# Kernel optimization log

Hardware: AMD Instinct MI355X
Metric: run time of the kernel (lower is better)

## Reference

```python
import jax, jax.numpy as jnp
import numpy as np

# Static feature-pyramid shapes (stride 8/16/32 of a 512x512 image)
SPATIAL_SHAPES = ((64, 64), (32, 32), (16, 16))
SEQ = sum(h * w for h, w in SPATIAL_SHAPES)  # 5376
B, D, NH, NL, NP = 4, 256, 8, 3, 4
DH = D // NH  # 32


def _reference_points():
    # normalized pixel centers per level, valid_ratios == 1
    refs = []
    for (h, w) in SPATIAL_SHAPES:
        ry = (jnp.arange(h, dtype=jnp.float32) + 0.5) / h
        rx = (jnp.arange(w, dtype=jnp.float32) + 0.5) / w
        yy, xx = jnp.meshgrid(ry, rx, indexing='ij')
        refs.append(jnp.stack([xx.reshape(-1), yy.reshape(-1)], -1))  # [h*w, 2]
    ref = jnp.concatenate(refs, 0)  # [S, 2]
    return jnp.broadcast_to(ref[None, :, None, :], (B, SEQ, NL, 2))


def setup_inputs() -> dict:
    key = jax.random.key(0)
    ks = jax.random.split(key, 8)
    s = 0.02
    return {
        'hidden_states': jax.random.normal(ks[0], (B, SEQ, D), jnp.float32),
        'position_embeddings': jax.random.normal(ks[1], (B, SEQ, D), jnp.float32),
        'reference_points': _reference_points(),
        'Wv': jax.random.normal(ks[2], (D, D), jnp.float32) * s,
        'bv': jnp.zeros((D,), jnp.float32),
        'Wo': jax.random.normal(ks[3], (D, NH * NL * NP * 2), jnp.float32) * s,
        'bo': jax.random.normal(ks[4], (NH * NL * NP * 2,), jnp.float32) * 0.1,
        'Wa': jax.random.normal(ks[5], (D, NH * NL * NP), jnp.float32) * s,
        'ba': jnp.zeros((NH * NL * NP,), jnp.float32),
        'Wout': jax.random.normal(ks[6], (D, D), jnp.float32) * s,
        'bout': jnp.zeros((D,), jnp.float32),
    }


def _bilinear_sample(img, gx, gy):
    # img: [N, C, H, W]; gx, gy: [N, Q, P] in [-1, 1]
    # grid_sample(mode='bilinear', padding_mode='zeros', align_corners=False)
    N, C, H, W = img.shape
    x = (gx + 1.0) * (W * 0.5) - 0.5
    y = (gy + 1.0) * (H * 0.5) - 0.5
    x0 = jnp.floor(x)
    y0 = jnp.floor(y)
    wx, wy = x - x0, y - y0
    flat = img.reshape(N, C, H * W)
    out = jnp.zeros((N, C) + gx.shape[1:], img.dtype)
    for xi, wxi in ((x0, 1.0 - wx), (x0 + 1.0, wx)):
        for yi, wyi in ((y0, 1.0 - wy), (y0 + 1.0, wy)):
            valid = (xi >= 0) & (xi < W) & (yi >= 0) & (yi < H)
            xc = jnp.clip(xi, 0, W - 1).astype(jnp.int32)
            yc = jnp.clip(yi, 0, H - 1).astype(jnp.int32)
            idx = (yc * W + xc).reshape(N, 1, -1)  # [N,1,Q*P]
            v = jnp.take_along_axis(flat, idx, axis=2).reshape(N, C, *gx.shape[1:])
            out = out + v * (wxi * wyi * valid.astype(img.dtype))[:, None]
    return out  # [N, C, Q, P]


def reference(hidden_states, position_embeddings, reference_points,
              Wv, bv, Wo, bo, Wa, ba, Wout, bout):
    hs = hidden_states + position_embeddings  # queries carry pos embed
    value = hidden_states @ Wv + bv           # value from raw encoder states
    value = value.reshape(B, SEQ, NH, DH)

    off = (hs @ Wo + bo).reshape(B, SEQ, NH, NL, NP, 2)
    attn = jax.nn.softmax((hs @ Wa + ba).reshape(B, SEQ, NH, NL * NP), -1)
    attn = attn.reshape(B, SEQ, NH, NL, NP)

    # offset normalizer: [W_l, H_l] per level
    norm = jnp.array([[w, h] for (h, w) in SPATIAL_SHAPES], jnp.float32)
    loc = reference_points[:, :, None, :, None, :] + off / norm[None, None, None, :, None, :]
    grid = 2.0 * loc - 1.0  # [B, Q, H, L, P, 2]

    sampled = []
    start = 0
    for lvl, (h, w) in enumerate(SPATIAL_SHAPES):
        v_l = value[:, start:start + h * w]  # [B, h*w, H, d]
        start += h * w
        v_l = v_l.transpose(0, 2, 3, 1).reshape(B * NH, DH, h, w)
        g_l = grid[:, :, :, lvl].transpose(0, 2, 1, 3, 4).reshape(B * NH, SEQ, NP, 2)
        sampled.append(_bilinear_sample(v_l, g_l[..., 0], g_l[..., 1]))  # [B*H,d,Q,P]
    sampled = jnp.stack(sampled, -2).reshape(B * NH, DH, SEQ, NL * NP)

    aw = attn.transpose(0, 2, 1, 3, 4).reshape(B * NH, 1, SEQ, NL * NP)
    out = (sampled * aw).sum(-1)                   # [B*H, d, Q]
    out = out.reshape(B, NH * DH, SEQ).transpose(0, 2, 1)  # [B, Q, D]
    out = out @ Wout + bout
    return out, attn
```

## Files before the change

### kernel.cpp

```cpp
#include <hip/hip_runtime.h>
#include <hip/hip_bf16.h>
#include <math.h>

#define BB 4
#define SEQ 5376
#define DD 256
#define NH 8
#define NL 3
#define NP 4
#define DH 32
#define MTOT (BB * SEQ)

typedef __attribute__((ext_vector_type(8))) short bf16x8;
typedef __attribute__((ext_vector_type(4))) float f32x4;

__device__ __forceinline__ ushort f2b(float f) {
    __hip_bfloat16 h = __float2bfloat16(f);
    return *reinterpret_cast<ushort*>(&h);
}

__global__ void prep_acts(const float4* __restrict__ h, const float4* __restrict__ p,
                          ushort4* __restrict__ hb, ushort4* __restrict__ hsb, int n4) {
    int i = blockIdx.x * blockDim.x + threadIdx.x;
    int stride = gridDim.x * blockDim.x;
    for (; i < n4; i += stride) {
        float4 a = h[i], b = p[i];
        ushort4 ua, us;
        ua.x = f2b(a.x); ua.y = f2b(a.y); ua.z = f2b(a.z); ua.w = f2b(a.w);
        us.x = f2b(a.x + b.x); us.y = f2b(a.y + b.y);
        us.z = f2b(a.z + b.z); us.w = f2b(a.w + b.w);
        hb[i] = ua;
        hsb[i] = us;
    }
}

__global__ __launch_bounds__(256) void prep_w(
    const float* __restrict__ Wv, const float* __restrict__ Wo,
    const float* __restrict__ Wa, const float* __restrict__ Wout,
    const float* __restrict__ bo, const float* __restrict__ ba,
    ushort* __restrict__ Wt, float* __restrict__ bcomb) {
    int row = blockIdx.x;
    int k = threadIdx.x;
    if (row == 800) {
        for (int i = k; i < 288; i += 256)
            bcomb[i] = (i < 192) ? bo[i] : ba[i - 192];
        return;
    }
    const float* src;
    int N, n;
    if (row < 256)      { src = Wv;   N = 256; n = row; }
    else if (row < 448) { src = Wo;   N = 192; n = row - 256; }
    else if (row < 544) { src = Wa;   N = 96;  n = row - 448; }
    else                { src = Wout; N = 256; n = row - 544; }
    float v = src[(size_t)k * N + n];
    Wt[(size_t)row * 256 + k] = f2b(v);
}

template<bool OBF>
__global__ __launch_bounds__(256) void gemm_mfma(
    const ushort* __restrict__ A, const ushort* __restrict__ Wt,
    const float* __restrict__ bias, void* __restrict__ Cout,
    int M, int N, int K) {
    const int BM = 128, BN = 64, BK = 64, PK = 72;
    __shared__ ushort As[BM][PK];
    __shared__ ushort Bs[BN][PK];
    int bm = blockIdx.y * BM;
    int bn = blockIdx.x * BN;
    int tid = threadIdx.x;
    int lane = tid & 63;
    int wid = tid >> 6;
    int wr = wid >> 1, wc = wid & 1;
    int lr = lane & 15;
    int kg = lane >> 4;

    f32x4 acc[4][2] = {};

    for (int k0 = 0; k0 < K; k0 += BK) {
        #pragma unroll
        for (int c = 0; c < 4; c++) {
            int e = tid + 256 * c;
            int row = e >> 3, q = e & 7;
            const ushort* src = A + (size_t)(bm + row) * K + k0 + 8 * q;
            *(bf16x8*)&As[row][8 * q] = *(const bf16x8*)src;
        }
        #pragma unroll
        for (int c = 0; c < 2; c++) {
            int e = tid + 256 * c;
            int row = e >> 3, q = e & 7;
            int gn = bn + row;
            bf16x8 v = {0, 0, 0, 0, 0, 0, 0, 0};
            if (gn < N) v = *(const bf16x8*)(Wt + (size_t)gn * K + k0 + 8 * q);
            *(bf16x8*)&Bs[row][8 * q] = v;
        }
        __syncthreads();
        #pragma unroll
        for (int ks = 0; ks < 2; ks++) {
            bf16x8 af[4], bfr[2];
            #pragma unroll
            for (int mf = 0; mf < 4; mf++)
                af[mf] = *(bf16x8*)&As[wr * 64 + mf * 16 + lr][ks * 32 + kg * 8];
            #pragma unroll
            for (int nf = 0; nf < 2; nf++)
                bfr[nf] = *(bf16x8*)&Bs[wc * 32 + nf * 16 + lr][ks * 32 + kg * 8];
            #pragma unroll
            for (int mf = 0; mf < 4; mf++)
                #pragma unroll
                for (int nf = 0; nf < 2; nf++)
                    acc[mf][nf] = __builtin_amdgcn_mfma_f32_16x16x32_bf16(
                        af[mf], bfr[nf], acc[mf][nf], 0, 0, 0);
        }
        __syncthreads();
    }

    #pragma unroll
    for (int nf = 0; nf < 2; nf++) {
        int gc = bn + wc * 32 + nf * 16 + lr;
        if (gc >= N) continue;
        float bv = bias[gc];
        #pragma unroll
        for (int mf = 0; mf < 4; mf++) {
            int gr0 = bm + wr * 64 + mf * 16 + kg * 4;
            #pragma unroll
            for (int r = 0; r < 4; r++) {
                float v = acc[mf][nf][r] + bv;
                if constexpr (OBF)
                    ((ushort*)Cout)[(size_t)(gr0 + r) * N + gc] = f2b(v);
                else
                    ((float*)Cout)[(size_t)(gr0 + r) * N + gc] = v;
            }
        }
    }
}

struct Acc8 {
    float a0, a1, a2, a3, a4, a5, a6, a7;
};

__device__ __forceinline__ void fma8(Acc8& acc, float wt, uint4 u) {
    acc.a0 = fmaf(wt, __uint_as_float(u.x << 16), acc.a0);
    acc.a1 = fmaf(wt, __uint_as_float(u.x & 0xffff0000u), acc.a1);
    acc.a2 = fmaf(wt, __uint_as_float(u.y << 16), acc.a2);
    acc.a3 = fmaf(wt, __uint_as_float(u.y & 0xffff0000u), acc.a3);
    acc.a4 = fmaf(wt, __uint_as_float(u.z << 16), acc.a4);
    acc.a5 = fmaf(wt, __uint_as_float(u.z & 0xffff0000u), acc.a5);
    acc.a6 = fmaf(wt, __uint_as_float(u.w << 16), acc.a6);
    acc.a7 = fmaf(wt, __uint_as_float(u.w & 0xffff0000u), acc.a7);
}

__global__ __launch_bounds__(128) void msda_sample_v7(
    const ushort* __restrict__ value, const float* __restrict__ comb,
    const float* __restrict__ refp, float* __restrict__ attn_out,
    ushort* __restrict__ out) {
    __shared__ int4   s_idx[4][8][13];
    __shared__ float4 s_w[4][8][13];
    int tid = threadIdx.x;
    int bq0 = blockIdx.x * 4;

    #pragma unroll
    for (int it = 0; it < 4; it++) {
        int t = tid + it * 128;
        int lp = t & 15;
        int qh = t >> 4;
        int q = qh >> 3, h = qh & 7;
        int bq = bq0 + q;
        bool active = lp < 12;
        const float* crow = comb + (size_t)bq * 288;
        float logit = active ? crow[192 + h * 12 + lp] : -INFINITY;
        float m = logit;
        m = fmaxf(m, __shfl_xor(m, 1, 16));
        m = fmaxf(m, __shfl_xor(m, 2, 16));
        m = fmaxf(m, __shfl_xor(m, 4, 16));
        m = fmaxf(m, __shfl_xor(m, 8, 16));
        float e = active ? expf(logit - m) : 0.f;
        float s = e;
        s += __shfl_xor(s, 1, 16);
        s += __shfl_xor(s, 2, 16);
        s += __shfl_xor(s, 4, 16);
        s += __shfl_xor(s, 8, 16);
        float aw = e / s;
        if (active) {
            attn_out[(size_t)bq * 96 + h * 12 + lp] = aw;
            int l = lp >> 2;
            int b = bq / SEQ;
            int Wl = 64 >> l;
            float fW = (float)Wl;
            float rx = refp[(size_t)bq * 6 + 2 * l];
            float ry = refp[(size_t)bq * 6 + 2 * l + 1];
            float ox = crow[h * 24 + lp * 2];
            float oy = crow[h * 24 + lp * 2 + 1];
            float x = rx * fW + ox - 0.5f;
            float y = ry * fW + oy - 0.5f;
            float x0f = floorf(x), y0f = floorf(y);
            float wx = x - x0f, wy = y - y0f;
            int x0 = (int)x0f, y0 = (int)y0f;
            int x1 = x0 + 1, y1 = y0 + 1;
            float vx0 = (x0 >= 0 && x0 < Wl) ? 1.f : 0.f;
            float vx1 = (x1 >= 0 && x1 < Wl) ? 1.f : 0.f;
            float vy0 = (y0 >= 0 && y0 < Wl) ? 1.f : 0.f;
            float vy1 = (y1 >= 0 && y1 < Wl) ? 1.f : 0.f;
            int xc0 = min(max(x0, 0), Wl - 1);
            int xc1 = min(max(x1, 0), Wl - 1);
            int yc0 = min(max(y0, 0), Wl - 1);
            int yc1 = min(max(y1, 0), Wl - 1);
            int st = (l == 0) ? 0 : ((l == 1) ? 4096 : 5120);
            int rowbase = b * SEQ + st;
            s_idx[q][h][lp] = make_int4((rowbase + yc0 * Wl + xc0) << 8,
                                        (rowbase + yc0 * Wl + xc1) << 8,
                                        (rowbase + yc1 * Wl + xc0) << 8,
                                        (rowbase + yc1 * Wl + xc1) << 8);
            s_w[q][h][lp] = make_float4(aw * (1.f - wx) * (1.f - wy) * vx0 * vy0,
                                        aw * wx * (1.f - wy) * vx1 * vy0,
                                        aw * (1.f - wx) * wy * vx0 * vy1,
                                        aw * wx * wy * vx1 * vy1);
        }
    }
    __syncthreads();

    int wave = tid >> 6, lane = tid & 63;
    int q2 = lane >> 5;
    int lane5 = lane & 31;
    int h = lane5 >> 2, d8 = lane5 & 3;
    int q = wave * 2 + q2;
    int bq = bq0 + q;
    int ch0 = h * 32 + d8 * 8;
    const ushort* vb = value + ch0;

    Acc8 acc = {0.f, 0.f, 0.f, 0.f, 0.f, 0.f, 0.f, 0.f};
    #pragma unroll
    for (int lp = 0; lp < 12; lp++) {
        int4 ii = s_idx[q][h][lp];
        float4 ww = s_w[q][h][lp];
        uint4 u0 = *(const uint4*)(vb + ii.x);
        uint4 u1 = *(const uint4*)(vb + ii.y);
        uint4 u2 = *(const uint4*)(vb + ii.z);
        uint4 u3 = *(const uint4*)(vb + ii.w);
        fma8(acc, ww.x, u0);
        fma8(acc, ww.y, u1);
        fma8(acc, ww.z, u2);
        fma8(acc, ww.w, u3);
    }

    bf16x8 o;
    o[0] = (short)f2b(acc.a0); o[1] = (short)f2b(acc.a1);
    o[2] = (short)f2b(acc.a2); o[3] = (short)f2b(acc.a3);
    o[4] = (short)f2b(acc.a4); o[5] = (short)f2b(acc.a5);
    o[6] = (short)f2b(acc.a6); o[7] = (short)f2b(acc.a7);
    *(bf16x8*)(out + (size_t)bq * 256 + ch0) = o;
}

extern "C" void kernel_launch(void* const* d_in, const int* in_sizes, int n_in,
                              void* d_out, int out_size, void* d_ws, size_t ws_size,
                              hipStream_t stream) {
    const float* hidden = (const float*)d_in[0];
    const float* pos    = (const float*)d_in[1];
    const float* refp   = (const float*)d_in[2];
    const float* Wv     = (const float*)d_in[3];
    const float* bv     = (const float*)d_in[4];
    const float* Wo     = (const float*)d_in[5];
    const float* bo     = (const float*)d_in[6];
    const float* Wa     = (const float*)d_in[7];
    const float* ba     = (const float*)d_in[8];
    const float* Wout   = (const float*)d_in[9];
    const float* bout   = (const float*)d_in[10];

    float* out      = (float*)d_out;
    float* attn_out = out + (size_t)BB * SEQ * DD;

    const size_t BSD = (size_t)BB * SEQ * DD;
    char* w = (char*)d_ws;
    ushort* value_bf = (ushort*)w;  w += BSD * 2;
    float*  comb     = (float*)w;   w += (size_t)MTOT * 288 * 4;
    ushort* sampb    = (ushort*)w;  w += BSD * 2;
    ushort* hb       = (ushort*)w;  w += BSD * 2;
    ushort* hsb      = (ushort*)w;  w += BSD * 2;
    ushort* Wt       = (ushort*)w;  w += (size_t)800 * 256 * 2;
    float*  bcomb    = (float*)w;

    {
        int n4 = (int)(BSD / 4);
        prep_acts<<<2048, 256, 0, stream>>>((const float4*)hidden, (const float4*)pos,
                                            (ushort4*)hb, (ushort4*)hsb, n4);
    }
    prep_w<<<801, 256, 0, stream>>>(Wv, Wo, Wa, Wout, bo, ba, Wt, bcomb);

    const ushort* Wv_t    = Wt;
    const ushort* Wcomb_t = Wt + (size_t)256 * 256;
    const ushort* Wout_t  = Wt + (size_t)544 * 256;

    {
        dim3 grid(DD / 64, MTOT / 128);
        gemm_mfma<true><<<grid, 256, 0, stream>>>(hb, Wv_t, bv, value_bf, MTOT, DD, DD);
    }
    {
        dim3 grid(5, MTOT / 128);
        gemm_mfma<false><<<grid, 256, 0, stream>>>(hsb, Wcomb_t, bcomb, comb, MTOT, 288, DD);
    }
    {
        msda_sample_v7<<<MTOT / 4, 128, 0, stream>>>(value_bf, comb, refp,
                                                     attn_out, sampb);
    }
    {
        dim3 grid(DD / 64, MTOT / 128);
        gemm_mfma<false><<<grid, 256, 0, stream>>>(sampb, Wout_t, bout, out, MTOT, DD, DD);
    }
}
```

Before: 94.18 us.

## Merge prep kernels, widen GEMM N-tile to 128, shrink sampler blocks

Merges the activation and weight conversion kernels into one launch, splitting the work by block index. The GEMM N-tile grows from 64 to 128, so each wave holds 4x4 MFMA accumulators and more output shares each A-tile load. The sampling kernel now uses single-wave 64-thread blocks that each handle two queries instead of four. Together these remove a launch and improve A-tile reuse, but the GEMMs launch fewer blocks, which use more registers, and the combined GEMM (N=288) wastes part of its third column tile.

Result: no change. 94.98 us (+0.8%).

```diff
diff --git a/kernel.cpp b/kernel.cpp
--- a/kernel.cpp
+++ b/kernel.cpp
@@ -19,12 +19,38 @@
     return *reinterpret_cast<ushort*>(&h);
 }
 
-__global__ void prep_acts(const float4* __restrict__ h, const float4* __restrict__ p,
-                          ushort4* __restrict__ hb, ushort4* __restrict__ hsb, int n4) {
-    int i = blockIdx.x * blockDim.x + threadIdx.x;
-    int stride = gridDim.x * blockDim.x;
+__global__ __launch_bounds__(256) void prep_all(
+    const float* __restrict__ hidden, const float* __restrict__ pos,
+    const float* __restrict__ Wv, const float* __restrict__ Wo,
+    const float* __restrict__ Wa, const float* __restrict__ Wout,
+    const float* __restrict__ bo, const float* __restrict__ ba,
+    ushort4* __restrict__ hb, ushort4* __restrict__ hsb,
+    ushort* __restrict__ Wt, float* __restrict__ bcomb, int n4) {
+    int bid = blockIdx.x;
+    int tid = threadIdx.x;
+    if (bid <= 800) {
+        if (bid == 800) {
+            for (int i = tid; i < 288; i += 256)
+                bcomb[i] = (i < 192) ? bo[i] : ba[i - 192];
+            return;
+        }
+        int row = bid;
+        const float* src;
+        int N, n;
+        if (row < 256)      { src = Wv;   N = 256; n = row; }
+        else if (row < 448) { src = Wo;   N = 192; n = row - 256; }
+        else if (row < 544) { src = Wa;   N = 96;  n = row - 448; }
+        else                { src = Wout; N = 256; n = row - 544; }
+        float v = src[(size_t)tid * N + n];
+        Wt[(size_t)row * 256 + tid] = f2b(v);
+        return;
+    }
+    const float4* h4 = (const float4*)hidden;
+    const float4* p4 = (const float4*)pos;
+    int i = (bid - 801) * 256 + tid;
+    int stride = (gridDim.x - 801) * 256;
     for (; i < n4; i += stride) {
-        float4 a = h[i], b = p[i];
+        float4 a = h4[i], b = p4[i];
         ushort4 ua, us;
         ua.x = f2b(a.x); ua.y = f2b(a.y); ua.z = f2b(a.z); ua.w = f2b(a.w);
         us.x = f2b(a.x + b.x); us.y = f2b(a.y + b.y);
@@ -34,34 +60,12 @@
     }
 }
 
-__global__ __launch_bounds__(256) void prep_w(
-    const float* __restrict__ Wv, const float* __restrict__ Wo,
-    const float* __restrict__ Wa, const float* __restrict__ Wout,
-    const float* __restrict__ bo, const float* __restrict__ ba,
-    ushort* __restrict__ Wt, float* __restrict__ bcomb) {
-    int row = blockIdx.x;
-    int k = threadIdx.x;
-    if (row == 800) {
-        for (int i = k; i < 288; i += 256)
-            bcomb[i] = (i < 192) ? bo[i] : ba[i - 192];
-        return;
-    }
-    const float* src;
-    int N, n;
-    if (row < 256)      { src = Wv;   N = 256; n = row; }
-    else if (row < 448) { src = Wo;   N = 192; n = row - 256; }
-    else if (row < 544) { src = Wa;   N = 96;  n = row - 448; }
-    else                { src = Wout; N = 256; n = row - 544; }
-    float v = src[(size_t)k * N + n];
-    Wt[(size_t)row * 256 + k] = f2b(v);
-}
-
 template<bool OBF>
 __global__ __launch_bounds__(256) void gemm_mfma(
     const ushort* __restrict__ A, const ushort* __restrict__ Wt,
     const float* __restrict__ bias, void* __restrict__ Cout,
     int M, int N, int K) {
-    const int BM = 128, BN = 64, BK = 64, PK = 72;
+    const int BM = 128, BN = 128, BK = 64, PK = 72;
     __shared__ ushort As[BM][PK];
     __shared__ ushort Bs[BN][PK];
     int bm = blockIdx.y * BM;
@@ -73,7 +77,7 @@
     int lr = lane & 15;
     int kg = lane >> 4;
 
-    f32x4 acc[4][2] = {};
+    f32x4 acc[4][4] = {};
 
     for (int k0 = 0; k0 < K; k0 += BK) {
         #pragma unroll
@@ -84,7 +88,7 @@
             *(bf16x8*)&As[row][8 * q] = *(const bf16x8*)src;
         }
         #pragma unroll
-        for (int c = 0; c < 2; c++) {
+        for (int c = 0; c < 4; c++) {
             int e = tid + 256 * c;
             int row = e >> 3, q = e & 7;
             int gn = bn + row;
@@ -95,17 +99,17 @@
         __syncthreads();
         #pragma unroll
         for (int ks = 0; ks < 2; ks++) {
-            bf16x8 af[4], bfr[2];
+            bf16x8 af[4], bfr[4];
             #pragma unroll
             for (int mf = 0; mf < 4; mf++)
                 af[mf] = *(bf16x8*)&As[wr * 64 + mf * 16 + lr][ks * 32 + kg * 8];
             #pragma unroll
-            for (int nf = 0; nf < 2; nf++)
-                bfr[nf] = *(bf16x8*)&Bs[wc * 32 + nf * 16 + lr][ks * 32 + kg * 8];
+            for (int nf = 0; nf < 4; nf++)
+                bfr[nf] = *(bf16x8*)&Bs[wc * 64 + nf * 16 + lr][ks * 32 + kg * 8];
             #pragma unroll
             for (int mf = 0; mf < 4; mf++)
                 #pragma unroll
-                for (int nf = 0; nf < 2; nf++)
+                for (int nf = 0; nf < 4; nf++)
                     acc[mf][nf] = __builtin_amdgcn_mfma_f32_16x16x32_bf16(
                         af[mf], bfr[nf], acc[mf][nf], 0, 0, 0);
         }
@@ -113,8 +117,8 @@
     }
 
     #pragma unroll
-    for (int nf = 0; nf < 2; nf++) {
-        int gc = bn + wc * 32 + nf * 16 + lr;
+    for (int nf = 0; nf < 4; nf++) {
+        int gc = bn + wc * 64 + nf * 16 + lr;
         if (gc >= N) continue;
         float bv = bias[gc];
         #pragma unroll
@@ -147,18 +151,18 @@
     acc.a7 = fmaf(wt, __uint_as_float(u.w & 0xffff0000u), acc.a7);
 }
 
-__global__ __launch_bounds__(128) void msda_sample_v7(
+__global__ __launch_bounds__(64) void msda_sample_v8(
     const ushort* __restrict__ value, const float* __restrict__ comb,
     const float* __restrict__ refp, float* __restrict__ attn_out,
     ushort* __restrict__ out) {
-    __shared__ int4   s_idx[4][8][13];
-    __shared__ float4 s_w[4][8][13];
+    __shared__ int4   s_idx[2][8][13];
+    __shared__ float4 s_w[2][8][13];
     int tid = threadIdx.x;
-    int bq0 = blockIdx.x * 4;
+    int bq0 = blockIdx.x * 2;
 
     #pragma unroll
     for (int it = 0; it < 4; it++) {
-        int t = tid + it * 128;
+        int t = tid + it * 64;
         int lp = t & 15;
         int qh = t >> 4;
         int q = qh >> 3, h = qh & 7;
@@ -216,11 +220,9 @@
     }
     __syncthreads();
 
-    int wave = tid >> 6, lane = tid & 63;
-    int q2 = lane >> 5;
-    int lane5 = lane & 31;
+    int q = tid >> 5;
+    int lane5 = tid & 31;
     int h = lane5 >> 2, d8 = lane5 & 3;
-    int q = wave * 2 + q2;
     int bq = bq0 + q;
     int ch0 = h * 32 + d8 * 8;
     const ushort* vb = value + ch0;
@@ -278,29 +280,29 @@
 
     {
         int n4 = (int)(BSD / 4);
-        prep_acts<<<2048, 256, 0, stream>>>((const float4*)hidden, (const float4*)pos,
-                                            (ushort4*)hb, (ushort4*)hsb, n4);
-    }
-    prep_w<<<801, 256, 0, stream>>>(Wv, Wo, Wa, Wout, bo, ba, Wt, bcomb);
+        prep_all<<<801 + 2048, 256, 0, stream>>>(hidden, pos, Wv, Wo, Wa, Wout,
+                                                 bo, ba, (ushort4*)hb, (ushort4*)hsb,
+                                                 Wt, bcomb, n4);
+    }
 
     const ushort* Wv_t    = Wt;
     const ushort* Wcomb_t = Wt + (size_t)256 * 256;
     const ushort* Wout_t  = Wt + (size_t)544 * 256;
 
     {
-        dim3 grid(DD / 64, MTOT / 128);
+        dim3 grid(DD / 128, MTOT / 128);
         gemm_mfma<true><<<grid, 256, 0, stream>>>(hb, Wv_t, bv, value_bf, MTOT, DD, DD);
     }
     {
-        dim3 grid(5, MTOT / 128);
+        dim3 grid(3, MTOT / 128);
         gemm_mfma<false><<<grid, 256, 0, stream>>>(hsb, Wcomb_t, bcomb, comb, MTOT, 288, DD);
     }
     {
-        msda_sample_v7<<<MTOT / 4, 128, 0, stream>>>(value_bf, comb, refp,
-                                                     attn_out, sampb);
-    }
-    {
-        dim3 grid(DD / 64, MTOT / 128);
+        msda_sample_v8<<<MTOT / 2, 64, 0, stream>>>(value_bf, comb, refp,
+                                                    attn_out, sampb);
+    }
+    {
+        dim3 grid(DD / 128, MTOT / 128);
         gemm_mfma<false><<<grid, 256, 0, stream>>>(sampb, Wout_t, bout, out, MTOT, DD, DD);
     }
 }
```
